# Kernel optimization log

Measured on AMD Instinct MI355X. Metric: run time of the kernel, lower is better.

Reference implementation:

```python
import jax, jax.numpy as jnp
import numpy as np

NUM_VERTS = 6890
NUM_JOINTS = 24
NUM_BETAS = 10
NUM_POSE_FEATS = 207  # 23 joints * 9
NUM_COCO_JOINTS = 19
BATCH = 1024

SMPL_PARENTS = np.array([0, 0, 0, 0, 1, 2, 3, 4, 5, 6, 7, 8, 9, 9, 9,
                         12, 13, 14, 16, 17, 18, 19, 20, 21], dtype=np.int32)


def batch_rodrigues(theta):
    """theta: [N,3] axis-angle -> [N,3,3] rotation matrices (Rodrigues)."""
    angle = jnp.linalg.norm(theta + 1e-8, axis=1, keepdims=True)  # [N,1]
    r = theta / angle                                             # [N,3]
    c = jnp.cos(angle)[:, :, None]                                # [N,1,1]
    s = jnp.sin(angle)[:, :, None]
    rx, ry, rz = r[:, 0], r[:, 1], r[:, 2]
    zeros = jnp.zeros_like(rx)
    K = jnp.stack([zeros, -rz, ry,
                   rz, zeros, -rx,
                   -ry, rx, zeros], axis=1).reshape(-1, 3, 3)     # skew(r)
    eye = jnp.eye(3, dtype=theta.dtype)
    return eye + s * K + (1.0 - c) * jnp.matmul(K, K)


def batch_global_rigid_transformation(Rs, Js, parents, rotate_base=True):
    """Rs: [B,24,3,3], Js: [B,24,3]. Returns (new_J [B,24,3], A [B,24,4,4])."""
    B = Rs.shape[0]
    dtype = Rs.dtype
    if rotate_base:
        rot_x = jnp.array([[1., 0., 0.], [0., -1., 0.], [0., 0., -1.]], dtype=dtype)
        root_rot = jnp.matmul(Rs[:, 0], rot_x)
    else:
        root_rot = Rs[:, 0]

    bottom = jnp.broadcast_to(jnp.array([0., 0., 0., 1.], dtype=dtype), (B, 1, 4))

    def make_A(R, t):  # R [B,3,3], t [B,3] -> [B,4,4]
        top = jnp.concatenate([R, t[:, :, None]], axis=2)  # [B,3,4]
        return jnp.concatenate([top, bottom], axis=1)

    results = [make_A(root_rot, Js[:, 0])]
    for i in range(1, NUM_JOINTS):
        t_rel = Js[:, i] - Js[:, parents[i]]
        A_here = make_A(Rs[:, i], t_rel)
        results.append(jnp.matmul(results[parents[i]], A_here))
    results = jnp.stack(results, axis=1)  # [B,24,4,4]

    new_J = results[:, :, :3, 3]
    # A = results - pad(results @ [J;0]) : subtract rotated rest joint from translation
    t_adj = jnp.einsum('bjpq,bjq->bjp', results[:, :, :3, :3], Js)  # [B,24,3]
    A = results.at[:, :, :3, 3].add(-t_adj)
    return new_J, A


def setup_inputs() -> dict:
    key = jax.random.key(0)
    ks = jax.random.split(key, 8)
    beta = jax.random.normal(ks[0], (BATCH, NUM_BETAS), dtype=jnp.float32)
    theta = jax.random.normal(ks[1], (BATCH, NUM_JOINTS * 3), dtype=jnp.float32) * 0.3
    v_template = jax.random.normal(ks[2], (NUM_VERTS, 3), dtype=jnp.float32)
    shapedirs = jax.random.normal(ks[3], (NUM_BETAS, NUM_VERTS * 3), dtype=jnp.float32) * 0.01
    J_regressor = jax.random.uniform(ks[4], (NUM_JOINTS, NUM_VERTS), dtype=jnp.float32) / NUM_VERTS
    posedirs = jax.random.normal(ks[5], (NUM_POSE_FEATS, NUM_VERTS * 3), dtype=jnp.float32) * 0.01
    joint_regressor = jax.random.uniform(ks[6], (NUM_COCO_JOINTS, NUM_VERTS), dtype=jnp.float32) / NUM_VERTS
    w_raw = jax.random.uniform(ks[7], (NUM_VERTS, NUM_JOINTS), dtype=jnp.float32)
    weights = w_raw / jnp.sum(w_raw, axis=1, keepdims=True)  # LBS weights, rows sum to 1
    parents = jnp.asarray(SMPL_PARENTS)
    return {"beta": beta, "theta": theta, "v_template": v_template,
            "shapedirs": shapedirs, "J_regressor": J_regressor,
            "posedirs": posedirs, "joint_regressor": joint_regressor,
            "weights": weights, "parents": parents}


def reference(beta, theta, v_template, shapedirs, J_regressor,
              posedirs, joint_regressor, weights, parents):
    B = beta.shape[0]
    parents_np = np.asarray(parents)

    # Shape blendshapes: [B,10]@[10,20670] -> [B,6890,3]
    v_shaped = jnp.matmul(beta, shapedirs).reshape(B, NUM_VERTS, 3) + v_template

    J = jnp.einsum('bvd,jv->bjd', v_shaped, J_regressor)

    # Pose rotations
    Rs = batch_rodrigues(theta.reshape(-1, 3)).reshape(B, NUM_JOINTS, 3, 3)
    pose_feature = (Rs[:, 1:] - jnp.eye(3, dtype=Rs.dtype)).reshape(B, NUM_POSE_FEATS)
    v_posed = jnp.matmul(pose_feature, posedirs).reshape(B, NUM_VERTS, 3) + v_shaped

    # Kinematic chain
    J_transformed, A = batch_global_rigid_transformation(Rs, J, parents_np, rotate_base=True)

    # Linear blend skinning: per-vertex 4x4 transforms
    T = jnp.einsum('vj,bjpq->bvpq', weights, A)  # [B,6890,4,4]
    ones = jnp.ones((B, NUM_VERTS, 1), dtype=v_posed.dtype)
    v_posed_homo = jnp.concatenate([v_posed, ones], axis=2)  # [B,6890,4]
    verts = jnp.einsum('bvpq,bvq->bvp', T[:, :, :3, :], v_posed_homo)  # [B,6890,3]

    joints = jnp.einsum('bvd,jv->bjd', verts, joint_regressor)  # [B,19,3]
    return verts, joints, Rs
```

## Files before the change

### kernel.cpp

```cpp
#include <hip/hip_runtime.h>
#include <math.h>

#define NV   6890
#define NJ   24
#define NB   10
#define NPF  207
#define NCJ  19
#define BATCHN 1024
#define NC3  (NV*3)
#define KTOT 224
#define NVP  6892

#define OUT_JOINTS_OFF (BATCHN*NV*3)
#define OUT_RS_OFF     (OUT_JOINTS_OFF + BATCHN*NCJ*3)

#define WS_JS     0
#define WS_EF     1024
#define WS_AADJT  115712
#define WS_JRB    377856
#define WS_DIRST  443392
#define WS_WTB    2765824
#define WS_END    2876416

typedef __attribute__((ext_vector_type(8))) short short8;
typedef __attribute__((ext_vector_type(4))) float f32x4;

__device__ __forceinline__ unsigned short f2bf(float f) {
    unsigned u = __float_as_uint(f);
    unsigned r = u + 0x7FFFu + ((u >> 16) & 1u);
    return (unsigned short)(r >> 16);
}
__device__ __forceinline__ float bf2f(unsigned short u) {
    return __uint_as_float((unsigned)u << 16);
}
__device__ __forceinline__ void async16(unsigned short* lds, const unsigned short* g) {
    __builtin_amdgcn_global_load_lds(
        (const __attribute__((address_space(1))) void*)g,
        (__attribute__((address_space(3))) void*)lds, 16, 0, 0);
}

__global__ __launch_bounds__(256) void smpl_kAP(
    const float* __restrict__ pdirs, const float* __restrict__ sdirs,
    unsigned short* __restrict__ dirsT,
    const float* __restrict__ jreg, const float* __restrict__ vtmpl,
    float* __restrict__ js,
    const float* __restrict__ jointreg, unsigned short* __restrict__ jrb,
    const float* __restrict__ wts, unsigned short* __restrict__ wtb) {
    int bx = blockIdx.x, t = threadIdx.x;
    if (bx < NJ) {
        int j = bx;
        float acc[33];
#pragma unroll
        for (int e = 0; e < 33; e++) acc[e] = 0.f;
        for (int v = t; v < NV; v += 256) {
            float w = jreg[j * NV + v];
#pragma unroll
            for (int k = 0; k < NB; k++) {
#pragma unroll
                for (int d = 0; d < 3; d++)
                    acc[k * 3 + d] += w * sdirs[(size_t)k * NC3 + v * 3 + d];
            }
#pragma unroll
            for (int d = 0; d < 3; d++) acc[30 + d] += w * vtmpl[v * 3 + d];
        }
#pragma unroll
        for (int e = 0; e < 33; e++) {
#pragma unroll
            for (int off = 32; off >= 1; off >>= 1) acc[e] += __shfl_xor(acc[e], off, 64);
        }
        __shared__ float red[4][33];
        int lane = t & 63, wv = t >> 6;
        if (lane == 0) {
#pragma unroll
            for (int e = 0; e < 33; e++) red[wv][e] = acc[e];
        }
        __syncthreads();
        if (t < 33) js[j * 33 + t] = red[0][t] + red[1][t] + red[2][t] + red[3][t];
        return;
    }
    if (bx < NJ + 216 * 6) {
        int b2 = bx - NJ;
        int vt = b2 / 6, part = b2 - (b2 / 6) * 6;
        for (int g = part * 448 + t; g < part * 448 + 448; g += 256) {
            int frag = g >> 6, fo = g & 63;
            int ks = frag / 6, s = frag - ks * 6;
            int l15 = fo >> 2, lg = fo & 3;
            int gc = vt * 96 + s * 16 + l15;
            int k0 = ks * 32 + lg * 8;
            unsigned short pk[8];
#pragma unroll
            for (int i = 0; i < 8; i++) {
                int k = k0 + i;
                float val = 0.f;
                if (gc < NC3) {
                    if (k < NPF) val = pdirs[(size_t)k * NC3 + gc];
                    else if (k < NPF + NB) val = sdirs[(size_t)(k - NPF) * NC3 + gc];
                    else if (k == NPF + NB) val = vtmpl[gc];
                }
                pk[i] = f2bf(val);
            }
            *(short8*)(dirsT + (size_t)vt * 21504 + (size_t)g * 8) = *(const short8*)pk;
        }
        return;
    }
    if (bx < NJ + 216 * 6 + NCJ) {
        int j = bx - (NJ + 216 * 6);
        for (int v = t; v < NVP; v += 256)
            jrb[(size_t)j * NVP + v] = (v < NV) ? f2bf(jointreg[(size_t)j * NV + v]) : 0;
        return;
    }
    int vt = bx - (NJ + 216 * 6 + NCJ);
    for (int e = t; e < 1024; e += 256) {
        int vl = e >> 5, k = e & 31;
        int gv = vt * 32 + vl;
        float w = (k < NJ && gv < NV) ? wts[(size_t)gv * NJ + k] : 0.f;
        wtb[(size_t)vt * 1024 + e] = f2bf(w);
    }
}

__global__ void smpl_kB(const float* __restrict__ theta, const float* __restrict__ beta_,
                        const float* __restrict__ js, float* __restrict__ outRs,
                        unsigned short* __restrict__ ef, unsigned short* __restrict__ aadjT) {
    int b = blockIdx.x;
    int t = threadIdx.x;
    __shared__ float Rl[NJ][9];
    __shared__ float Jl[NJ][3];
    __shared__ float Rw[NJ][12];

    if (t < NJ) {
        int j = t;
        float tx = theta[b * 72 + j * 3 + 0];
        float ty = theta[b * 72 + j * 3 + 1];
        float tz = theta[b * 72 + j * 3 + 2];
        float ax = tx + 1e-8f, ay = ty + 1e-8f, az = tz + 1e-8f;
        float ang = sqrtf(ax * ax + ay * ay + az * az);
        float inv = 1.0f / ang;
        float rx = tx * inv, ry = ty * inv, rz = tz * inv;
        float s = sinf(ang), c = cosf(ang), t1 = 1.0f - c;
        float R[9];
        R[0] = 1.0f - t1 * (ry * ry + rz * rz);
        R[1] = -s * rz + t1 * rx * ry;
        R[2] =  s * ry + t1 * rx * rz;
        R[3] =  s * rz + t1 * rx * ry;
        R[4] = 1.0f - t1 * (rx * rx + rz * rz);
        R[5] = -s * rx + t1 * ry * rz;
        R[6] = -s * ry + t1 * rx * rz;
        R[7] =  s * rx + t1 * ry * rz;
        R[8] = 1.0f - t1 * (rx * rx + ry * ry);
#pragma unroll
        for (int e = 0; e < 9; e++) {
            Rl[j][e] = R[e];
            outRs[(size_t)b * 216 + j * 9 + e] = R[e];
        }
#pragma unroll
        for (int d = 0; d < 3; d++) {
            float accJ = js[j * 33 + 30 + d];
#pragma unroll
            for (int k = 0; k < NB; k++) accJ += beta_[b * NB + k] * js[j * 33 + k * 3 + d];
            Jl[j][d] = accJ;
        }
    }
    __syncthreads();
    for (int e = t; e < KTOT; e += 64) {
        float val;
        if (e < NPF) {
            int j = e / 9 + 1;
            int rc = e - (j - 1) * 9;
            val = Rl[j][rc] - ((rc == 0 || rc == 4 || rc == 8) ? 1.0f : 0.0f);
        } else if (e < NPF + NB) {
            val = beta_[b * NB + (e - NPF)];
        } else if (e == NPF + NB) {
            val = 1.0f;
        } else val = 0.f;
        ef[(size_t)b * KTOT + e] = f2bf(val);
    }
    if (t == 0) {
#pragma unroll
        for (int r = 0; r < 3; r++) {
            Rw[0][r * 4 + 0] =  Rl[0][r * 3 + 0];
            Rw[0][r * 4 + 1] = -Rl[0][r * 3 + 1];
            Rw[0][r * 4 + 2] = -Rl[0][r * 3 + 2];
            Rw[0][r * 4 + 3] =  Jl[0][r];
        }
        const int par[NJ] = {0,0,0,0,1,2,3,4,5,6,7,8,9,9,9,12,13,14,16,17,18,19,20,21};
#pragma unroll
        for (int i = 1; i < NJ; i++) {
            int p = par[i];
            float tr0 = Jl[i][0] - Jl[p][0];
            float tr1 = Jl[i][1] - Jl[p][1];
            float tr2 = Jl[i][2] - Jl[p][2];
#pragma unroll
            for (int r = 0; r < 3; r++) {
                float p0 = Rw[p][r * 4 + 0], p1 = Rw[p][r * 4 + 1], p2 = Rw[p][r * 4 + 2];
#pragma unroll
                for (int cc = 0; cc < 3; cc++)
                    Rw[i][r * 4 + cc] = p0 * Rl[i][0 + cc] + p1 * Rl[i][3 + cc] + p2 * Rl[i][6 + cc];
                Rw[i][r * 4 + 3] = p0 * tr0 + p1 * tr1 + p2 * tr2 + Rw[p][r * 4 + 3];
            }
        }
    }
    __syncthreads();
    for (int i = t; i < 512; i += 64) {
        int n = i >> 5, k = i & 31;
        float v = 0.f;
        if (n < 12 && k < 24) {
            int r = n >> 2, cc = n & 3;
            if (cc < 3) v = Rw[k][n];
            else v = Rw[k][r * 4 + 3] - (Rw[k][r * 4 + 0] * Jl[k][0] + Rw[k][r * 4 + 1] * Jl[k][1] +
                                         Rw[k][r * 4 + 2] * Jl[k][2]);
        }
        aadjT[(size_t)b * 512 + i] = f2bf(v);
    }
}

__global__ __launch_bounds__(512, 2) void smpl_kC11(
    const unsigned short* __restrict__ dirsT, const unsigned short* __restrict__ wtb,
    const unsigned short* __restrict__ ef, const unsigned short* __restrict__ aadjT,
    float* __restrict__ outv) {
    __shared__ __align__(16) unsigned short Bb[2][21504];
    __shared__ __align__(16) unsigned short Wt[2][1024];
    __shared__ __align__(16) unsigned short vph[8][2176];

    int tid = threadIdx.x;
    int cg = blockIdx.x;
    int bt = blockIdx.y;
    int lane = tid & 63, wv = tid >> 6;
    int l15 = lane & 15, lg = lane >> 4;
    int fo = l15 * 4 + lg;
    int nvt = (cg < 24) ? 7 : 6;
    int bb = bt * 128 + wv * 16;

    const unsigned short* efb = ef + (size_t)(bb + l15) * KTOT;
    short8 av[7];
#pragma unroll
    for (int ks = 0; ks < 7; ks++) av[ks] = *(const short8*)(efb + ks * 32 + lg * 8);
    const short8* at0 = (const short8*)(aadjT + (size_t)bb * 512);
    short8 afr[16];
#pragma unroll
    for (int i = 0; i < 16; i++) afr[i] = at0[i * 64 + fo];

    auto stage = [&](int i, int p) {
        int vt = cg + i * 32;
        const unsigned short* bsrc = dirsT + (size_t)vt * 21504;
        for (int g0 = wv * 64; g0 < 2688; g0 += 512)
            async16(&Bb[p][(size_t)g0 * 8], bsrc + ((size_t)g0 + lane) * 8);
        if (wv < 2) {
            int g0 = wv * 64;
            async16(&Wt[p][g0 * 8], wtb + (size_t)vt * 1024 + ((size_t)g0 + lane) * 8);
        }
    };

    stage(0, 0);
    __syncthreads();

    unsigned short* vp = vph[wv];

    for (int i = 0; i < nvt; i++) {
        int pc = i & 1;
        if (i + 1 < nvt) stage(i + 1, pc ^ 1);
        int vt = cg + i * 32;

        short8 wf0 = *(const short8*)&Wt[pc][l15 * 32 + lg * 8];
        short8 wf1 = *(const short8*)&Wt[pc][(16 + l15) * 32 + lg * 8];

        f32x4 acc[6];
#pragma unroll
        for (int s = 0; s < 6; s++) acc[s] = (f32x4){0.f, 0.f, 0.f, 0.f};
#pragma unroll
        for (int ks = 0; ks < 7; ks++) {
#pragma unroll
            for (int s = 0; s < 6; s++) {
                short8 bv = *(const short8*)&Bb[pc][((ks * 6 + s) << 9) + fo * 8];
                acc[s] = __builtin_amdgcn_mfma_f32_16x16x32_bf16(av[ks], bv, acc[s], 0, 0, 0);
            }
        }
#pragma unroll
        for (int s = 0; s < 6; s++) {
            int col = s * 16 + l15;
            int v = col / 3, d = col - v * 3;
#pragma unroll
            for (int r = 0; r < 4; r++)
                vp[(v * 17 + lg * 4 + r) * 4 + d] = f2bf(acc[s][r]);
        }
#pragma unroll
        for (int bl2 = 0; bl2 < 16; bl2++) {
            short8 af = afr[bl2];
            f32x4 z = (f32x4){0.f, 0.f, 0.f, 0.f};
            f32x4 t0 = __builtin_amdgcn_mfma_f32_16x16x32_bf16(af, wf0, z, 0, 0, 0);
            f32x4 t1 = __builtin_amdgcn_mfma_f32_16x16x32_bf16(af, wf1, z, 0, 0, 0);
            int b = bb + bl2;
            if (lg < 3) {
                int p = lg;
                {
                    int vv = l15;
                    ushort4 xv = *(const ushort4*)&vp[(vv * 17 + bl2) * 4];
                    float o = fmaf(t0[0], bf2f(xv.x),
                              fmaf(t0[1], bf2f(xv.y), fmaf(t0[2], bf2f(xv.z), t0[3])));
                    int gv = vt * 32 + vv;
                    if (gv < NV) outv[(size_t)b * NC3 + gv * 3 + p] = o;
                }
                {
                    int vv = 16 + l15;
                    ushort4 xv = *(const ushort4*)&vp[(vv * 17 + bl2) * 4];
                    float o = fmaf(t1[0], bf2f(xv.x),
                              fmaf(t1[1], bf2f(xv.y), fmaf(t1[2], bf2f(xv.z), t1[3])));
                    int gv = vt * 32 + vv;
                    if (gv < NV) outv[(size_t)b * NC3 + gv * 3 + p] = o;
                }
            }
        }
        __syncthreads();
    }
}

__global__ __launch_bounds__(256) void smpl_kD(
    const float* __restrict__ verts, const unsigned short* __restrict__ jrb,
    float* __restrict__ outj) {
    int tid = threadIdx.x;
    int b = blockIdx.x;
    const float* vb = verts + (size_t)b * NC3;
    float acc[57];
#pragma unroll
    for (int e = 0; e < 57; e++) acc[e] = 0.f;

    for (int it = 0; it < 7; it++) {
        int g = it * 256 + tid;
        if (g < 1723) {
            int v = g * 4;
            const float* pa = vb + v * 3;
            float2 q0 = *(const float2*)(pa + 0);
            float2 q1 = *(const float2*)(pa + 2);
            float2 q2 = *(const float2*)(pa + 4);
            float2 q3 = *(const float2*)(pa + 6);
            float2 q4 = *(const float2*)(pa + 8);
            float2 q5 = *(const float2*)(pa + 10);
#pragma unroll
            for (int j = 0; j < NCJ; j++) {
                uint2 wp = *(const uint2*)(jrb + (size_t)j * NVP + v);
                float w0 = __uint_as_float((wp.x & 0xFFFFu) << 16);
                float w1 = __uint_as_float(wp.x & 0xFFFF0000u);
                float w2 = __uint_as_float((wp.y & 0xFFFFu) << 16);
                float w3 = __uint_as_float(wp.y & 0xFFFF0000u);
                acc[j * 3 + 0] += w0 * q0.x + w1 * q1.y + w2 * q3.x + w3 * q4.y;
                acc[j * 3 + 1] += w0 * q0.y + w1 * q2.x + w2 * q3.y + w3 * q5.x;
                acc[j * 3 + 2] += w0 * q1.x + w1 * q2.y + w2 * q4.x + w3 * q5.y;
            }
        }
    }
#pragma unroll
    for (int e = 0; e < 57; e++) {
#pragma unroll
        for (int off = 32; off >= 1; off >>= 1) acc[e] += __shfl_xor(acc[e], off, 64);
    }
    __shared__ float red[4][57];
    int lane = tid & 63, wv = tid >> 6;
    if (lane == 0) {
#pragma unroll
        for (int e = 0; e < 57; e++) red[wv][e] = acc[e];
    }
    __syncthreads();
    if (tid < 57)
        outj[(size_t)b * 57 + tid] = red[0][tid] + red[1][tid] + red[2][tid] + red[3][tid];
}

extern "C" void kernel_launch(void* const* d_in, const int* in_sizes, int n_in,
                              void* d_out, int out_size, void* d_ws, size_t ws_size,
                              hipStream_t stream) {
    (void)in_sizes; (void)n_in; (void)out_size; (void)ws_size;
    const float* beta       = (const float*)d_in[0];
    const float* theta      = (const float*)d_in[1];
    const float* v_template = (const float*)d_in[2];
    const float* shapedirs  = (const float*)d_in[3];
    const float* jreg       = (const float*)d_in[4];
    const float* posedirs   = (const float*)d_in[5];
    const float* jointreg   = (const float*)d_in[6];
    const float* weights    = (const float*)d_in[7];
    float* out = (float*)d_out;
    float* ws  = (float*)d_ws;
    unsigned short* ef    = (unsigned short*)(ws + WS_EF);
    unsigned short* aadjT = (unsigned short*)(ws + WS_AADJT);
    unsigned short* jrb   = (unsigned short*)(ws + WS_JRB);
    unsigned short* dirsT = (unsigned short*)(ws + WS_DIRST);
    unsigned short* wtb   = (unsigned short*)(ws + WS_WTB);

    smpl_kAP<<<NJ + 216 * 6 + NCJ + 216, 256, 0, stream>>>(
        posedirs, shapedirs, dirsT, jreg, v_template, ws + WS_JS,
        jointreg, jrb, weights, wtb);
    smpl_kB<<<BATCHN, 64, 0, stream>>>(theta, beta, ws + WS_JS, out + OUT_RS_OFF,
                                       ef, aadjT);
    dim3 gC(32, 8);
    smpl_kC11<<<gC, 512, 0, stream>>>(dirsT, wtb, ef, aadjT, out);
    smpl_kD<<<BATCHN, 256, 0, stream>>>(out, jrb, out + OUT_JOINTS_OFF);
}
```

Baseline: 114.4 us.

## Fuse joint regression into skinning kernel via MFMA and atomic accumulation

Removes the separate joint-regression kernel, which re-read all output vertices from global memory. The skinning kernel now writes bf16 copies of its skinned vertices back into LDS. It multiplies them against a per-tile transposed bf16 joint regressor with MFMA, accumulates per-block partial joints in registers, and atomically adds them into the output, which kB zeroes first. This saves a launch and a full pass over the vertex output, at the cost of bf16 rounding of the vertices, extra MFMA/LDS work inside the hot loop, and float atomics.

Result: slower. 170.6 us (+49.1%).

```diff
diff --git a/kernel.cpp b/kernel.cpp
--- a/kernel.cpp
+++ b/kernel.cpp
@@ -9,7 +9,6 @@
 #define BATCHN 1024
 #define NC3  (NV*3)
 #define KTOT 224
-#define NVP  6892
 
 #define OUT_JOINTS_OFF (BATCHN*NV*3)
 #define OUT_RS_OFF     (OUT_JOINTS_OFF + BATCHN*NCJ*3)
@@ -17,10 +16,10 @@
 #define WS_JS     0
 #define WS_EF     1024
 #define WS_AADJT  115712
-#define WS_JRB    377856
 #define WS_DIRST  443392
 #define WS_WTB    2765824
-#define WS_END    2876416
+#define WS_JRTB   2876416
+#define WS_END    2987008
 
 typedef __attribute__((ext_vector_type(8))) short short8;
 typedef __attribute__((ext_vector_type(4))) float f32x4;
@@ -44,7 +43,7 @@
     unsigned short* __restrict__ dirsT,
     const float* __restrict__ jreg, const float* __restrict__ vtmpl,
     float* __restrict__ js,
-    const float* __restrict__ jointreg, unsigned short* __restrict__ jrb,
+    const float* __restrict__ jointreg, unsigned short* __restrict__ jrtb,
     const float* __restrict__ wts, unsigned short* __restrict__ wtb) {
     int bx = blockIdx.x, t = threadIdx.x;
     if (bx < NJ) {
@@ -103,29 +102,33 @@
         }
         return;
     }
-    if (bx < NJ + 216 * 6 + NCJ) {
-        int j = bx - (NJ + 216 * 6);
-        for (int v = t; v < NVP; v += 256)
-            jrb[(size_t)j * NVP + v] = (v < NV) ? f2bf(jointreg[(size_t)j * NV + v]) : 0;
-        return;
-    }
-    int vt = bx - (NJ + 216 * 6 + NCJ);
+    int vt = bx - (NJ + 216 * 6);
     for (int e = t; e < 1024; e += 256) {
         int vl = e >> 5, k = e & 31;
         int gv = vt * 32 + vl;
         float w = (k < NJ && gv < NV) ? wts[(size_t)gv * NJ + k] : 0.f;
         wtb[(size_t)vt * 1024 + e] = f2bf(w);
     }
+    for (int e = t; e < 1024; e += 256) {
+        int h = e >> 9, rem = e & 511, jj = rem >> 5, k = rem & 31;
+        int j2 = h * 16 + jj;
+        int gv = vt * 32 + k;
+        float w = (j2 < NCJ && gv < NV) ? jointreg[(size_t)j2 * NV + gv] : 0.f;
+        jrtb[(size_t)vt * 1024 + e] = f2bf(w);
+    }
 }
 
 __global__ void smpl_kB(const float* __restrict__ theta, const float* __restrict__ beta_,
                         const float* __restrict__ js, float* __restrict__ outRs,
-                        unsigned short* __restrict__ ef, unsigned short* __restrict__ aadjT) {
+                        unsigned short* __restrict__ ef, unsigned short* __restrict__ aadjT,
+                        float* __restrict__ outj) {
     int b = blockIdx.x;
     int t = threadIdx.x;
     __shared__ float Rl[NJ][9];
     __shared__ float Jl[NJ][3];
     __shared__ float Rw[NJ][12];
+
+    if (t < 57) outj[(size_t)b * 57 + t] = 0.f;
 
     if (t < NJ) {
         int j = t;
@@ -213,10 +216,11 @@
     }
 }
 
-__global__ __launch_bounds__(512, 2) void smpl_kC11(
+__global__ __launch_bounds__(512, 2) void smpl_kC15(
     const unsigned short* __restrict__ dirsT, const unsigned short* __restrict__ wtb,
-    const unsigned short* __restrict__ ef, const unsigned short* __restrict__ aadjT,
-    float* __restrict__ outv) {
+    const unsigned short* __restrict__ jrtb, const unsigned short* __restrict__ ef,
+    const unsigned short* __restrict__ aadjT, float* __restrict__ outv,
+    float* __restrict__ outj) {
     __shared__ __align__(16) unsigned short Bb[2][21504];
     __shared__ __align__(16) unsigned short Wt[2][1024];
     __shared__ __align__(16) unsigned short vph[8][2176];
@@ -239,6 +243,13 @@
 #pragma unroll
     for (int i = 0; i < 16; i++) afr[i] = at0[i * 64 + fo];
 
+    f32x4 aj0[3], aj1[3];
+#pragma unroll
+    for (int d = 0; d < 3; d++) {
+        aj0[d] = (f32x4){0.f, 0.f, 0.f, 0.f};
+        aj1[d] = (f32x4){0.f, 0.f, 0.f, 0.f};
+    }
+
     auto stage = [&](int i, int p) {
         int vt = cg + i * 32;
         const unsigned short* bsrc = dirsT + (size_t)vt * 21504;
@@ -262,6 +273,9 @@
 
         short8 wf0 = *(const short8*)&Wt[pc][l15 * 32 + lg * 8];
         short8 wf1 = *(const short8*)&Wt[pc][(16 + l15) * 32 + lg * 8];
+        const short8* jrp = (const short8*)(jrtb + (size_t)vt * 1024);
+        short8 ja0 = jrp[fo];
+        short8 ja1 = jrp[64 + fo];
 
         f32x4 acc[6];
 #pragma unroll
@@ -291,76 +305,47 @@
             int b = bb + bl2;
             if (lg < 3) {
                 int p = lg;
-                {
-                    int vv = l15;
-                    ushort4 xv = *(const ushort4*)&vp[(vv * 17 + bl2) * 4];
-                    float o = fmaf(t0[0], bf2f(xv.x),
-                              fmaf(t0[1], bf2f(xv.y), fmaf(t0[2], bf2f(xv.z), t0[3])));
-                    int gv = vt * 32 + vv;
-                    if (gv < NV) outv[(size_t)b * NC3 + gv * 3 + p] = o;
-                }
-                {
-                    int vv = 16 + l15;
-                    ushort4 xv = *(const ushort4*)&vp[(vv * 17 + bl2) * 4];
-                    float o = fmaf(t1[0], bf2f(xv.x),
-                              fmaf(t1[1], bf2f(xv.y), fmaf(t1[2], bf2f(xv.z), t1[3])));
-                    int gv = vt * 32 + vv;
-                    if (gv < NV) outv[(size_t)b * NC3 + gv * 3 + p] = o;
-                }
-            }
+                int vv0 = l15, vv1 = 16 + l15;
+                ushort4 xa = *(const ushort4*)&vp[(vv0 * 17 + bl2) * 4];
+                ushort4 xb = *(const ushort4*)&vp[(vv1 * 17 + bl2) * 4];
+                float o0 = fmaf(t0[0], bf2f(xa.x),
+                           fmaf(t0[1], bf2f(xa.y), fmaf(t0[2], bf2f(xa.z), t0[3])));
+                float o1 = fmaf(t1[0], bf2f(xb.x),
+                           fmaf(t1[1], bf2f(xb.y), fmaf(t1[2], bf2f(xb.z), t1[3])));
+                vp[(vv0 * 17 + bl2) * 4 + p] = f2bf(o0);
+                vp[(vv1 * 17 + bl2) * 4 + p] = f2bf(o1);
+                int gv0 = vt * 32 + vv0, gv1 = vt * 32 + vv1;
+                if (gv0 < NV) outv[(size_t)b * NC3 + gv0 * 3 + p] = o0;
+                if (gv1 < NV) outv[(size_t)b * NC3 + gv1 * 3 + p] = o1;
+            }
+        }
+#pragma unroll
+        for (int d = 0; d < 3; d++) {
+            unsigned short bvv[8];
+#pragma unroll
+            for (int q = 0; q < 8; q++)
+                bvv[q] = vp[((lg * 8 + q) * 17 + l15) * 4 + d];
+            short8 bq = *(const short8*)bvv;
+            aj0[d] = __builtin_amdgcn_mfma_f32_16x16x32_bf16(ja0, bq, aj0[d], 0, 0, 0);
+            aj1[d] = __builtin_amdgcn_mfma_f32_16x16x32_bf16(ja1, bq, aj1[d], 0, 0, 0);
         }
         __syncthreads();
     }
-}
-
-__global__ __launch_bounds__(256) void smpl_kD(
-    const float* __restrict__ verts, const unsigned short* __restrict__ jrb,
-    float* __restrict__ outj) {
-    int tid = threadIdx.x;
-    int b = blockIdx.x;
-    const float* vb = verts + (size_t)b * NC3;
-    float acc[57];
-#pragma unroll
-    for (int e = 0; e < 57; e++) acc[e] = 0.f;
-
-    for (int it = 0; it < 7; it++) {
-        int g = it * 256 + tid;
-        if (g < 1723) {
-            int v = g * 4;
-            const float* pa = vb + v * 3;
-            float2 q0 = *(const float2*)(pa + 0);
-            float2 q1 = *(const float2*)(pa + 2);
-            float2 q2 = *(const float2*)(pa + 4);
-            float2 q3 = *(const float2*)(pa + 6);
-            float2 q4 = *(const float2*)(pa + 8);
-            float2 q5 = *(const float2*)(pa + 10);
-#pragma unroll
-            for (int j = 0; j < NCJ; j++) {
-                uint2 wp = *(const uint2*)(jrb + (size_t)j * NVP + v);
-                float w0 = __uint_as_float((wp.x & 0xFFFFu) << 16);
-                float w1 = __uint_as_float(wp.x & 0xFFFF0000u);
-                float w2 = __uint_as_float((wp.y & 0xFFFFu) << 16);
-                float w3 = __uint_as_float(wp.y & 0xFFFF0000u);
-                acc[j * 3 + 0] += w0 * q0.x + w1 * q1.y + w2 * q3.x + w3 * q4.y;
-                acc[j * 3 + 1] += w0 * q0.y + w1 * q2.x + w2 * q3.y + w3 * q5.x;
-                acc[j * 3 + 2] += w0 * q1.x + w1 * q2.y + w2 * q4.x + w3 * q5.y;
-            }
-        }
-    }
-#pragma unroll
-    for (int e = 0; e < 57; e++) {
-#pragma unroll
-        for (int off = 32; off >= 1; off >>= 1) acc[e] += __shfl_xor(acc[e], off, 64);
-    }
-    __shared__ float red[4][57];
-    int lane = tid & 63, wv = tid >> 6;
-    if (lane == 0) {
-#pragma unroll
-        for (int e = 0; e < 57; e++) red[wv][e] = acc[e];
-    }
-    __syncthreads();
-    if (tid < 57)
-        outj[(size_t)b * 57 + tid] = red[0][tid] + red[1][tid] + red[2][tid] + red[3][tid];
+
+    int bj = bb + l15;
+#pragma unroll
+    for (int r = 0; r < 4; r++) {
+        int j0 = lg * 4 + r;
+#pragma unroll
+        for (int d = 0; d < 3; d++)
+            atomicAdd(&outj[(size_t)bj * 57 + j0 * 3 + d], aj0[d][r]);
+        int j1 = 16 + j0;
+        if (j1 < NCJ) {
+#pragma unroll
+            for (int d = 0; d < 3; d++)
+                atomicAdd(&outj[(size_t)bj * 57 + j1 * 3 + d], aj1[d][r]);
+        }
+    }
 }
 
 extern "C" void kernel_launch(void* const* d_in, const int* in_sizes, int n_in,
@@ -379,16 +364,16 @@
     float* ws  = (float*)d_ws;
     unsigned short* ef    = (unsigned short*)(ws + WS_EF);
     unsigned short* aadjT = (unsigned short*)(ws + WS_AADJT);
-    unsigned short* jrb   = (unsigned short*)(ws + WS_JRB);
     unsigned short* dirsT = (unsigned short*)(ws + WS_DIRST);
     unsigned short* wtb   = (unsigned short*)(ws + WS_WTB);
-
-    smpl_kAP<<<NJ + 216 * 6 + NCJ + 216, 256, 0, stream>>>(
+    unsigned short* jrtb  = (unsigned short*)(ws + WS_JRTB);
+
+    smpl_kAP<<<NJ + 216 * 6 + 216, 256, 0, stream>>>(
         posedirs, shapedirs, dirsT, jreg, v_template, ws + WS_JS,
-        jointreg, jrb, weights, wtb);
+        jointreg, jrtb, weights, wtb);
     smpl_kB<<<BATCHN, 64, 0, stream>>>(theta, beta, ws + WS_JS, out + OUT_RS_OFF,
-                                       ef, aadjT);
+                                       ef, aadjT, out + OUT_JOINTS_OFF);
     dim3 gC(32, 8);
-    smpl_kC11<<<gC, 512, 0, stream>>>(dirsT, wtb, ef, aadjT, out);
-    smpl_kD<<<BATCHN, 256, 0, stream>>>(out, jrb, out + OUT_JOINTS_OFF);
-}
+    smpl_kC15<<<gC, 512, 0, stream>>>(dirsT, wtb, jrtb, ef, aadjT, out,
+                                      out + OUT_JOINTS_OFF);
+}
```
